# Kernel tuning notes

Hardware: AMD Instinct MI355X
Metric: run time of the kernel (lower is better)

## Reference

```python
import jax, jax.numpy as jnp
import numpy as np

N_NODES = 50000
N_EDGES = 800000
D_IN, D_HID, D_OUT = 256, 128, 64
NEG_SLOPE = 0.2  # PyG GATConv default


def gat_conv(x, W, a_src, a_dst, b, src, dst, n):
    """Single-head PyG-style GATConv with self-loops already in (src, dst)."""
    h = x @ W                                  # [N, d_out]
    # per-edge attention logits: LeakyReLU(a_src . h_src + a_dst . h_dst)
    e = jax.nn.leaky_relu((h @ a_src)[src] + (h @ a_dst)[dst], NEG_SLOPE)  # [E]
    # segment softmax over incoming edges of each dst node (stable)
    e = e - jax.ops.segment_max(e, dst, num_segments=n)[dst]
    p = jnp.exp(e)
    p = p / jax.ops.segment_sum(p, dst, num_segments=n)[dst]
    # weighted scatter-add of source messages
    out = jax.ops.segment_sum(p[:, None] * h[src], dst, num_segments=n)
    return out + b


def setup_inputs() -> dict:
    key = jax.random.key(0)
    ks = jax.random.split(key, 10)
    x = jax.random.normal(ks[0], (N_NODES, D_IN), dtype=jnp.float32)
    edge_index = jax.random.randint(ks[1], (2, N_EDGES), 0, N_NODES, dtype=jnp.int32)
    s1 = 1.0 / np.sqrt(D_IN)
    s2 = 1.0 / np.sqrt(D_HID)
    W1 = jax.random.normal(ks[2], (D_IN, D_HID), dtype=jnp.float32) * s1
    a_src1 = jax.random.normal(ks[3], (D_HID,), dtype=jnp.float32) * s2
    a_dst1 = jax.random.normal(ks[4], (D_HID,), dtype=jnp.float32) * s2
    b1 = jnp.zeros((D_HID,), dtype=jnp.float32)
    W2 = jax.random.normal(ks[5], (D_HID, D_OUT), dtype=jnp.float32) * s2
    a_src2 = jax.random.normal(ks[6], (D_OUT,), dtype=jnp.float32) * (1.0 / np.sqrt(D_OUT))
    a_dst2 = jax.random.normal(ks[7], (D_OUT,), dtype=jnp.float32) * (1.0 / np.sqrt(D_OUT))
    b2 = jnp.zeros((D_OUT,), dtype=jnp.float32)
    return {"x": x, "edge_index": edge_index, "W1": W1, "a_src1": a_src1,
            "a_dst1": a_dst1, "b1": b1, "W2": W2, "a_src2": a_src2,
            "a_dst2": a_dst2, "b2": b2}


def reference(x, edge_index, W1, a_src1, a_dst1, b1, W2, a_src2, a_dst2, b2):
    n = x.shape[0]
    loops = jnp.arange(n, dtype=edge_index.dtype)
    src = jnp.concatenate([edge_index[0], loops])  # add_self_loops=True (PyG default)
    dst = jnp.concatenate([edge_index[1], loops])
    h = gat_conv(x, W1, a_src1, a_dst1, b1, src, dst, n)
    h = jax.nn.relu(h)
    return gat_conv(h, W2, a_src2, a_dst2, b2, src, dst, n)
```

## Files before the change

kernel.cpp:

```cpp
#include <hip/hip_runtime.h>
#include <stdint.h>

#define DIN 256
#define DHID 128
#define DOUTD 64
#define NBLK 128
#define BCAP 4096

typedef __attribute__((ext_vector_type(8))) short bf16x8;
typedef __attribute__((ext_vector_type(4))) float f32x4;

__device__ __forceinline__ uint32_t pack_bf16x2(float x, float y) {
    uint32_t ux = __builtin_bit_cast(uint32_t, x);
    uint32_t uy = __builtin_bit_cast(uint32_t, y);
    ux += 0x7fffu + ((ux >> 16) & 1u);
    uy += 0x7fffu + ((uy >> 16) & 1u);
    return (ux >> 16) | (uy & 0xffff0000u);
}
__device__ __forceinline__ uint16_t to_bf16(float x) {
    uint32_t u = __builtin_bit_cast(uint32_t, x);
    u += 0x7fffu + ((u >> 16) & 1u);
    return (uint16_t)(u >> 16);
}
__device__ __forceinline__ float bflo(uint32_t v) { return __builtin_bit_cast(float, v << 16); }
__device__ __forceinline__ float bfhi(uint32_t v) { return __builtin_bit_cast(float, v & 0xffff0000u); }

template<int K, int N>
__device__ __forceinline__ void prepack_body(
    const float* __restrict__ W, uint16_t* __restrict__ Bp, int t)
{
    constexpr int CB = N / 16;
    if (t >= (K / 32) * CB * 64) return;
    const int lane = t & 63, fi = t >> 6;
    const int c = fi % CB, kb = fi / CB;
    const int j  = 16 * c + (lane & 15);
    const int k0 = kb * 32 + (lane >> 4) * 8;
    uint32_t o[4];
    #pragma unroll
    for (int i = 0; i < 4; ++i) {
        float lo = W[(size_t)(k0 + 2 * i)     * N + j];
        float hi = W[(size_t)(k0 + 2 * i + 1) * N + j];
        o[i] = pack_bf16x2(lo, hi);
    }
    *reinterpret_cast<uint4*>(&Bp[(size_t)t * 8]) = make_uint4(o[0], o[1], o[2], o[3]);
}

__global__ __launch_bounds__(256) void prepack_both_kernel(
    const float* __restrict__ W1, uint16_t* __restrict__ Bp1,
    const float* __restrict__ W2, uint16_t* __restrict__ Bp2,
    int* __restrict__ cntG, int nbuck)
{
    if (blockIdx.x == 0) {
        for (int i = threadIdx.x; i < nbuck; i += 256) cntG[i] = 0;
    }
    if (blockIdx.x < 16)
        prepack_body<DIN, DHID>(W1, Bp1, blockIdx.x * 256 + threadIdx.x);
    else
        prepack_body<DHID, DOUTD>(W2, Bp2, (blockIdx.x - 16) * 256 + threadIdx.x);
}

template<int K, int N, bool AF32>
__global__ __launch_bounds__(256) void mfma_gemm(
    const void* __restrict__ A, const uint16_t* __restrict__ Bp,
    uint16_t* __restrict__ Cout, const float* __restrict__ a_s,
    const float* __restrict__ a_d, float* __restrict__ asrc,
    float* __restrict__ adst, int M)
{
    constexpr int KB = K / 32, CB = N / 16;
    __shared__ __align__(16) uint16_t As[64 * K];

    const int tid = threadIdx.x;
    const int row0 = blockIdx.x * 64;

    if (AF32) {
        constexpr int NIT = 64 * K / 4 / 256;
        #pragma unroll
        for (int i = 0; i < NIT; ++i) {
            int u = tid + i * 256;
            int row = u / (K / 4);
            int k4  = (u % (K / 4)) * 4;
            float4 v = make_float4(0.f, 0.f, 0.f, 0.f);
            if (row0 + row < M)
                v = *reinterpret_cast<const float4*>((const float*)A + (size_t)(row0 + row) * K + k4);
            uint32_t byte = (uint32_t)row * (K * 2) + k4 * 2;
            byte ^= (row & 7) << 4;
            *reinterpret_cast<uint2*>((char*)As + byte) =
                make_uint2(pack_bf16x2(v.x, v.y), pack_bf16x2(v.z, v.w));
        }
    } else {
        constexpr int NIT = 64 * K / 8 / 256;
        #pragma unroll
        for (int i = 0; i < NIT; ++i) {
            int u = tid + i * 256;
            int row = u / (K / 8);
            int k8  = (u % (K / 8)) * 8;
            uint4 v = make_uint4(0u, 0u, 0u, 0u);
            if (row0 + row < M)
                v = *reinterpret_cast<const uint4*>((const uint16_t*)A + (size_t)(row0 + row) * K + k8);
            uint32_t byte = (uint32_t)row * (K * 2) + k8 * 2;
            byte ^= (row & 7) << 4;
            *reinterpret_cast<uint4*>((char*)As + byte) = v;
        }
    }
    __syncthreads();

    const int w = tid >> 6, l = tid & 63;
    const int rA = w * 16 + (l & 15);

    f32x4 acc[CB] = {};
    const char* blane = (const char*)Bp + l * 16;

    #pragma unroll
    for (int kb = 0; kb < KB; ++kb) {
        uint32_t abyte = (uint32_t)rA * (K * 2) + (kb * 32 + (l >> 4) * 8) * 2;
        abyte ^= (rA & 7) << 4;
        bf16x8 a = *reinterpret_cast<const bf16x8*>((const char*)As + abyte);
        #pragma unroll
        for (int c = 0; c < CB; ++c) {
            bf16x8 b = *reinterpret_cast<const bf16x8*>(blane + (size_t)(kb * CB + c) * 1024);
            acc[c] = __builtin_amdgcn_mfma_f32_16x16x32_bf16(a, b, acc[c], 0, 0, 0);
        }
    }

    const int rb = w * 16 + (l >> 4) * 4;
    const int colb = l & 15;

    #pragma unroll
    for (int c = 0; c < CB; ++c) {
        #pragma unroll
        for (int r = 0; r < 4; ++r) {
            int grow = row0 + rb + r;
            if (grow < M)
                Cout[(size_t)grow * N + c * 16 + colb] = to_bf16(acc[c][r]);
        }
    }

    float ps[4] = {}, pd[4] = {};
    #pragma unroll
    for (int c = 0; c < CB; ++c) {
        float asv = a_s[c * 16 + colb];
        float adv = a_d[c * 16 + colb];
        #pragma unroll
        for (int r = 0; r < 4; ++r) {
            ps[r] += acc[c][r] * asv;
            pd[r] += acc[c][r] * adv;
        }
    }
    #pragma unroll
    for (int mask = 1; mask < 16; mask <<= 1) {
        #pragma unroll
        for (int r = 0; r < 4; ++r) {
            ps[r] += __shfl_xor(ps[r], mask);
            pd[r] += __shfl_xor(pd[r], mask);
        }
    }
    if (colb == 0) {
        #pragma unroll
        for (int r = 0; r < 4; ++r) {
            int grow = row0 + rb + r;
            if (grow < M) { asrc[grow] = ps[r]; adst[grow] = pd[r]; }
        }
    }
}

__global__ __launch_bounds__(256) void histscatter_kernel(
    const int* __restrict__ ei, int E, int n, int nbuck, int chunk,
    int* __restrict__ cntG, uint32_t* __restrict__ bucketed)
{
    __shared__ int h[512];
    __shared__ int curL[512];
    for (int i = threadIdx.x; i < nbuck; i += 256) h[i] = 0;
    __syncthreads();
    const int blk = blockIdx.x;
    const int ET = E + n;
    const int e0 = blk * chunk, e1 = min(e0 + chunk, ET);
    for (int e = e0 + threadIdx.x; e < e1; e += 256) {
        int d = (e < E) ? ei[E + e] : (e - E);
        atomicAdd(&h[d >> 7], 1);
    }
    __syncthreads();
    for (int i = threadIdx.x; i < nbuck; i += 256) {
        int c = h[i];
        int base = i * BCAP;
        if (c) base += atomicAdd(&cntG[i], c);
        curL[i] = base;
    }
    __syncthreads();
    for (int e = e0 + threadIdx.x; e < e1; e += 256) {
        int s, d;
        if (e < E) { s = ei[e]; d = ei[E + e]; }
        else       { s = e - E; d = s; }
        int pos = atomicAdd(&curL[d >> 7], 1);
        bucketed[pos] = ((uint32_t)d << 16) | (uint32_t)s;
    }
}

__global__ __launch_bounds__(256) void csrF_kernel(
    const uint32_t* __restrict__ bucketed, const int* __restrict__ cntG,
    int n, int* __restrict__ offs, int* __restrict__ degs, int* __restrict__ csr)
{
    __shared__ int hist[128];
    __shared__ int scn[128];
    __shared__ int cur[128];
    const int b = blockIdx.x;
    const int tid = threadIdx.x;
    const int beg = b * BCAP;
    const int end = beg + cntG[b];

    if (tid < 128) hist[tid] = 0;
    __syncthreads();
    for (int i = beg + tid; i < end; i += 256)
        atomicAdd(&hist[(bucketed[i] >> 16) & 127], 1);
    __syncthreads();
    if (tid < 128) scn[tid] = hist[tid];
    __syncthreads();
    #pragma unroll
    for (int off = 1; off < 128; off <<= 1) {
        int v = (tid < 128 && tid >= off) ? scn[tid - off] : 0;
        __syncthreads();
        if (tid < 128) scn[tid] += v;
        __syncthreads();
    }
    if (tid < 128) {
        int excl = (tid == 0) ? 0 : scn[tid - 1];
        cur[tid] = beg + excl;
        int node = b * 128 + tid;
        if (node < n) { offs[node] = beg + excl; degs[node] = hist[tid]; }
    }
    __syncthreads();
    for (int i = beg + tid; i < end; i += 256) {
        uint32_t pk = bucketed[i];
        int pos = atomicAdd(&cur[(pk >> 16) & 127], 1);
        csr[pos] = (int)(pk & 0xFFFFu);
    }
}

template<int D, bool RELU, bool OUTB16>
__global__ __launch_bounds__(256) void agg_kernel(
    const uint32_t* __restrict__ Hb, const float* __restrict__ asrc,
    const float* __restrict__ adst, const int* __restrict__ offs,
    const int* __restrict__ degs, const int* __restrict__ csr_src,
    const float* __restrict__ bias, void* __restrict__ out, int n)
{
    constexpr int C16 = D / 8;
    constexpr int EPI = 64 / C16;
    const int wid = threadIdx.x >> 6, lane = threadIdx.x & 63;
    const int node = blockIdx.x * 4 + wid;
    if (node >= n) return;

    const int beg = offs[node];
    const int deg = degs[node];
    const float ad = adst[node];
    const int seg = lane / C16;
    const int chk = lane & (C16 - 1);
    const uint4* __restrict__ H4 = reinterpret_cast<const uint4*>(Hb);

    float acc[8] = {};
    float ssum = 0.f;

    for (int base = 0; base < deg; base += 64) {
        const int lim = min(64, deg - base);
        float wt = 0.f; int st = 0;
        if (lane < lim) {
            st = csr_src[beg + base + lane];
            float t = asrc[st] + ad;
            t = (t > 0.f) ? t : 0.2f * t;
            wt = __expf(t);
        }
        ssum += wt;
        const int iters = (lim + 2 * EPI - 1) / (2 * EPI);
        #pragma unroll 2
        for (int it = 0; it < iters; ++it) {
            int e0 = it * 2 * EPI + seg;
            int e1 = e0 + EPI;
            float w0 = __shfl(wt, e0);
            int   s0 = __shfl(st, e0);
            float w1 = __shfl(wt, e1);
            int   s1 = __shfl(st, e1);
            uint4 v0 = H4[(size_t)s0 * (D / 8) + chk];
            uint4 v1 = H4[(size_t)s1 * (D / 8) + chk];
            acc[0] += w0 * bflo(v0.x); acc[1] += w0 * bfhi(v0.x);
            acc[2] += w0 * bflo(v0.y); acc[3] += w0 * bfhi(v0.y);
            acc[4] += w0 * bflo(v0.z); acc[5] += w0 * bfhi(v0.z);
            acc[6] += w0 * bflo(v0.w); acc[7] += w0 * bfhi(v0.w);
            acc[0] += w1 * bflo(v1.x); acc[1] += w1 * bfhi(v1.x);
            acc[2] += w1 * bflo(v1.y); acc[3] += w1 * bfhi(v1.y);
            acc[4] += w1 * bflo(v1.z); acc[5] += w1 * bfhi(v1.z);
            acc[6] += w1 * bflo(v1.w); acc[7] += w1 * bfhi(v1.w);
        }
    }

    #pragma unroll
    for (int mask = C16; mask < 64; mask <<= 1)
        #pragma unroll
        for (int j = 0; j < 8; ++j)
            acc[j] += __shfl_xor(acc[j], mask);
    #pragma unroll
    for (int off = 32; off; off >>= 1) ssum += __shfl_xor(ssum, off);
    const float inv = 1.f / ssum;

    if (seg == 0) {
        const int col0 = chk * 8;
        float r[8];
        #pragma unroll
        for (int j = 0; j < 8; ++j) {
            r[j] = acc[j] * inv + bias[col0 + j];
            if (RELU) r[j] = fmaxf(r[j], 0.f);
        }
        if (OUTB16) {
            uint4 o = make_uint4(pack_bf16x2(r[0], r[1]), pack_bf16x2(r[2], r[3]),
                                 pack_bf16x2(r[4], r[5]), pack_bf16x2(r[6], r[7]));
            *(reinterpret_cast<uint4*>(out) + (size_t)node * (D / 8) + chk) = o;
        } else {
            float* op = (float*)out + (size_t)node * D + col0;
            *reinterpret_cast<float4*>(op)     = make_float4(r[0], r[1], r[2], r[3]);
            *reinterpret_cast<float4*>(op + 4) = make_float4(r[4], r[5], r[6], r[7]);
        }
    }
}

extern "C" void kernel_launch(void* const* d_in, const int* in_sizes, int n_in,
                              void* d_out, int out_size, void* d_ws, size_t ws_size,
                              hipStream_t stream)
{
    const float* x   = (const float*)d_in[0];
    const int*   ei  = (const int*)  d_in[1];
    const float* W1  = (const float*)d_in[2];
    const float* as1 = (const float*)d_in[3];
    const float* ad1 = (const float*)d_in[4];
    const float* b1  = (const float*)d_in[5];
    const float* W2  = (const float*)d_in[6];
    const float* as2 = (const float*)d_in[7];
    const float* ad2 = (const float*)d_in[8];
    const float* b2  = (const float*)d_in[9];
    float* out = (float*)d_out;

    const int n  = in_sizes[0] / DIN;
    const int E  = in_sizes[1] / 2;
    const int ET = E + n;

    const int nbuck  = (n + 127) >> 7;
    const int chunk  = (ET + NBLK - 1) / NBLK;

    char* ws = (char*)d_ws;
    size_t off = 0;
    auto alloc = [&](size_t bytes) -> void* {
        off = (off + 255) & ~(size_t)255;
        void* p = ws + off;
        off += bytes;
        return p;
    };
    uint16_t* Hb   = (uint16_t*)alloc((size_t)n * DHID * 2);
    uint16_t* O1b  = (uint16_t*)alloc((size_t)n * DHID * 2);
    uint16_t* H2b  = (uint16_t*)alloc((size_t)n * DOUTD * 2);
    float* asrc    = (float*)alloc((size_t)n * 4);
    float* adst    = (float*)alloc((size_t)n * 4);
    uint16_t* Bp1  = (uint16_t*)alloc((size_t)DIN * DHID * 2);
    uint16_t* Bp2  = (uint16_t*)alloc((size_t)DHID * DOUTD * 2);
    int* cntG  = (int*)alloc((size_t)nbuck * 4);
    int* offs  = (int*)alloc((size_t)n * 4);
    int* degs  = (int*)alloc((size_t)n * 4);
    uint32_t* bucketed = (uint32_t*)alloc((size_t)nbuck * BCAP * 4);
    int* csr   = (int*)alloc((size_t)nbuck * BCAP * 4);

    const int nw = (n + 3) / 4;
    const int ng = (n + 63) / 64;

    prepack_both_kernel<<<20, 256, 0, stream>>>(W1, Bp1, W2, Bp2, cntG, nbuck);

    histscatter_kernel<<<NBLK, 256, 0, stream>>>(ei, E, n, nbuck, chunk, cntG, bucketed);
    csrF_kernel<<<nbuck, 256, 0, stream>>>(bucketed, cntG, n, offs, degs, csr);

    mfma_gemm<DIN, DHID, true><<<ng, 256, 0, stream>>>(x, Bp1, Hb, as1, ad1, asrc, adst, n);
    agg_kernel<DHID, true, true><<<nw, 256, 0, stream>>>(
        (const uint32_t*)Hb, asrc, adst, offs, degs, csr, b1, O1b, n);

    mfma_gemm<DHID, DOUTD, false><<<ng, 256, 0, stream>>>(O1b, Bp2, H2b, as2, ad2, asrc, adst, n);
    agg_kernel<DOUTD, false, false><<<nw, 256, 0, stream>>>(
        (const uint32_t*)H2b, asrc, adst, offs, degs, csr, b2, out, n);
}
```

Baseline: 221.5 us.

## Fuse edge bucketing with layer-1 GEMM and build per-bucket CSR inside aggregation

The edge histogram/scatter pass and the first dense GEMM now run as one hybrid launch, with blocks split by index, so the two independent stages can overlap on the device. The separate CSR-finalize kernel is removed. Each aggregation block of 1024 threads instead sorts its 128-node bucket into a shared-memory CSR of 16-bit source indices, then processes those nodes with 16 waves. This cuts launches and global CSR/offset/degree traffic, and the local sort is repeated for both layers. It trades node-level parallelism in aggregation for larger blocks, fewer of them (about 391), and heavier LDS use, and the 16-bit indices cap the source id range.

```diff
diff --git a/kernel.cpp b/kernel.cpp
--- a/kernel.cpp
+++ b/kernel.cpp
@@ -60,17 +60,16 @@
 }
 
 template<int K, int N, bool AF32>
-__global__ __launch_bounds__(256) void mfma_gemm(
+__device__ __forceinline__ void gemm_body(
+    uint16_t* __restrict__ As,
     const void* __restrict__ A, const uint16_t* __restrict__ Bp,
     uint16_t* __restrict__ Cout, const float* __restrict__ a_s,
     const float* __restrict__ a_d, float* __restrict__ asrc,
-    float* __restrict__ adst, int M)
+    float* __restrict__ adst, int M, int bid)
 {
     constexpr int KB = K / 32, CB = N / 16;
-    __shared__ __align__(16) uint16_t As[64 * K];
-
     const int tid = threadIdx.x;
-    const int row0 = blockIdx.x * 64;
+    const int row0 = bid * 64;
 
     if (AF32) {
         constexpr int NIT = 64 * K / 4 / 256;
@@ -163,54 +162,84 @@
     }
 }
 
-__global__ __launch_bounds__(256) void histscatter_kernel(
+__global__ __launch_bounds__(256) void hybrid_kernel(
     const int* __restrict__ ei, int E, int n, int nbuck, int chunk,
-    int* __restrict__ cntG, uint32_t* __restrict__ bucketed)
-{
+    int* __restrict__ cntG, uint32_t* __restrict__ bucketed,
+    const float* __restrict__ x, const uint16_t* __restrict__ Bp1,
+    uint16_t* __restrict__ Hb, const float* __restrict__ a_s,
+    const float* __restrict__ a_d, float* __restrict__ asrc,
+    float* __restrict__ adst)
+{
+    __shared__ __align__(16) uint16_t As[64 * DIN];
     __shared__ int h[512];
     __shared__ int curL[512];
-    for (int i = threadIdx.x; i < nbuck; i += 256) h[i] = 0;
-    __syncthreads();
-    const int blk = blockIdx.x;
-    const int ET = E + n;
-    const int e0 = blk * chunk, e1 = min(e0 + chunk, ET);
-    for (int e = e0 + threadIdx.x; e < e1; e += 256) {
-        int d = (e < E) ? ei[E + e] : (e - E);
-        atomicAdd(&h[d >> 7], 1);
-    }
-    __syncthreads();
-    for (int i = threadIdx.x; i < nbuck; i += 256) {
-        int c = h[i];
-        int base = i * BCAP;
-        if (c) base += atomicAdd(&cntG[i], c);
-        curL[i] = base;
-    }
-    __syncthreads();
-    for (int e = e0 + threadIdx.x; e < e1; e += 256) {
-        int s, d;
-        if (e < E) { s = ei[e]; d = ei[E + e]; }
-        else       { s = e - E; d = s; }
-        int pos = atomicAdd(&curL[d >> 7], 1);
-        bucketed[pos] = ((uint32_t)d << 16) | (uint32_t)s;
-    }
-}
-
-__global__ __launch_bounds__(256) void csrF_kernel(
+
+    if (blockIdx.x < NBLK) {
+        for (int i = threadIdx.x; i < nbuck; i += 256) h[i] = 0;
+        __syncthreads();
+        const int blk = blockIdx.x;
+        const int ET = E + n;
+        const int e0 = blk * chunk, e1 = min(e0 + chunk, ET);
+        for (int e = e0 + threadIdx.x; e < e1; e += 256) {
+            int d = (e < E) ? ei[E + e] : (e - E);
+            atomicAdd(&h[d >> 7], 1);
+        }
+        __syncthreads();
+        for (int i = threadIdx.x; i < nbuck; i += 256) {
+            int c = h[i];
+            int base = i * BCAP;
+            if (c) base += atomicAdd(&cntG[i], c);
+            curL[i] = base;
+        }
+        __syncthreads();
+        for (int e = e0 + threadIdx.x; e < e1; e += 256) {
+            int s, d;
+            if (e < E) { s = ei[e]; d = ei[E + e]; }
+            else       { s = e - E; d = s; }
+            int pos = atomicAdd(&curL[d >> 7], 1);
+            bucketed[pos] = ((uint32_t)d << 16) | (uint32_t)s;
+        }
+    } else {
+        gemm_body<DIN, DHID, true>(As, x, Bp1, Hb, a_s, a_d, asrc, adst, n,
+                                   blockIdx.x - NBLK);
+    }
+}
+
+__global__ __launch_bounds__(256) void gemm2_kernel(
+    const uint16_t* __restrict__ A, const uint16_t* __restrict__ Bp,
+    uint16_t* __restrict__ Cout, const float* __restrict__ a_s,
+    const float* __restrict__ a_d, float* __restrict__ asrc,
+    float* __restrict__ adst, int M)
+{
+    __shared__ __align__(16) uint16_t As[64 * DHID];
+    gemm_body<DHID, DOUTD, false>(As, A, Bp, Cout, a_s, a_d, asrc, adst, M,
+                                  blockIdx.x);
+}
+
+template<int D, bool RELU, bool OUTB16>
+__global__ __launch_bounds__(1024) void aggF_kernel(
     const uint32_t* __restrict__ bucketed, const int* __restrict__ cntG,
-    int n, int* __restrict__ offs, int* __restrict__ degs, int* __restrict__ csr)
-{
+    const uint32_t* __restrict__ Hb, const float* __restrict__ asrc,
+    const float* __restrict__ adst, const float* __restrict__ bias,
+    void* __restrict__ out, int n)
+{
+    constexpr int C16 = D / 8;
+    constexpr int EPI = 64 / C16;
+    __shared__ uint16_t csr_l[BCAP];
     __shared__ int hist[128];
     __shared__ int scn[128];
+    __shared__ int offs_l[128];
     __shared__ int cur[128];
+
     const int b = blockIdx.x;
     const int tid = threadIdx.x;
-    const int beg = b * BCAP;
-    const int end = beg + cntG[b];
+    const int bbase = b * BCAP;
+    const int cnt = cntG[b];
 
     if (tid < 128) hist[tid] = 0;
     __syncthreads();
-    for (int i = beg + tid; i < end; i += 256)
-        atomicAdd(&hist[(bucketed[i] >> 16) & 127], 1);
+    for (int i = tid; i < cnt; i += 1024)
+        atomicAdd(&hist[(bucketed[bbase + i] >> 16) & 127], 1);
     __syncthreads();
     if (tid < 128) scn[tid] = hist[tid];
     __syncthreads();
@@ -222,99 +251,92 @@
         __syncthreads();
     }
     if (tid < 128) {
-        int excl = (tid == 0) ? 0 : scn[tid - 1];
-        cur[tid] = beg + excl;
-        int node = b * 128 + tid;
-        if (node < n) { offs[node] = beg + excl; degs[node] = hist[tid]; }
-    }
-    __syncthreads();
-    for (int i = beg + tid; i < end; i += 256) {
-        uint32_t pk = bucketed[i];
+        int excl = scn[tid] - hist[tid];
+        offs_l[tid] = excl;
+        cur[tid] = excl;
+    }
+    __syncthreads();
+    for (int i = tid; i < cnt; i += 1024) {
+        uint32_t pk = bucketed[bbase + i];
         int pos = atomicAdd(&cur[(pk >> 16) & 127], 1);
-        csr[pos] = (int)(pk & 0xFFFFu);
-    }
-}
-
-template<int D, bool RELU, bool OUTB16>
-__global__ __launch_bounds__(256) void agg_kernel(
-    const uint32_t* __restrict__ Hb, const float* __restrict__ asrc,
-    const float* __restrict__ adst, const int* __restrict__ offs,
-    const int* __restrict__ degs, const int* __restrict__ csr_src,
-    const float* __restrict__ bias, void* __restrict__ out, int n)
-{
-    constexpr int C16 = D / 8;
-    constexpr int EPI = 64 / C16;
-    const int wid = threadIdx.x >> 6, lane = threadIdx.x & 63;
-    const int node = blockIdx.x * 4 + wid;
-    if (node >= n) return;
-
-    const int beg = offs[node];
-    const int deg = degs[node];
-    const float ad = adst[node];
+        csr_l[pos] = (uint16_t)(pk & 0xFFFFu);
+    }
+    __syncthreads();
+
+    const int wv = tid >> 6, lane = tid & 63;
     const int seg = lane / C16;
     const int chk = lane & (C16 - 1);
     const uint4* __restrict__ H4 = reinterpret_cast<const uint4*>(Hb);
 
-    float acc[8] = {};
-    float ssum = 0.f;
-
-    for (int base = 0; base < deg; base += 64) {
-        const int lim = min(64, deg - base);
-        float wt = 0.f; int st = 0;
-        if (lane < lim) {
-            st = csr_src[beg + base + lane];
-            float t = asrc[st] + ad;
-            t = (t > 0.f) ? t : 0.2f * t;
-            wt = __expf(t);
-        }
-        ssum += wt;
-        const int iters = (lim + 2 * EPI - 1) / (2 * EPI);
-        #pragma unroll 2
-        for (int it = 0; it < iters; ++it) {
-            int e0 = it * 2 * EPI + seg;
-            int e1 = e0 + EPI;
-            float w0 = __shfl(wt, e0);
-            int   s0 = __shfl(st, e0);
-            float w1 = __shfl(wt, e1);
-            int   s1 = __shfl(st, e1);
-            uint4 v0 = H4[(size_t)s0 * (D / 8) + chk];
-            uint4 v1 = H4[(size_t)s1 * (D / 8) + chk];
-            acc[0] += w0 * bflo(v0.x); acc[1] += w0 * bfhi(v0.x);
-            acc[2] += w0 * bflo(v0.y); acc[3] += w0 * bfhi(v0.y);
-            acc[4] += w0 * bflo(v0.z); acc[5] += w0 * bfhi(v0.z);
-            acc[6] += w0 * bflo(v0.w); acc[7] += w0 * bfhi(v0.w);
-            acc[0] += w1 * bflo(v1.x); acc[1] += w1 * bfhi(v1.x);
-            acc[2] += w1 * bflo(v1.y); acc[3] += w1 * bfhi(v1.y);
-            acc[4] += w1 * bflo(v1.z); acc[5] += w1 * bfhi(v1.z);
-            acc[6] += w1 * bflo(v1.w); acc[7] += w1 * bfhi(v1.w);
-        }
-    }
-
-    #pragma unroll
-    for (int mask = C16; mask < 64; mask <<= 1)
-        #pragma unroll
-        for (int j = 0; j < 8; ++j)
-            acc[j] += __shfl_xor(acc[j], mask);
-    #pragma unroll
-    for (int off = 32; off; off >>= 1) ssum += __shfl_xor(ssum, off);
-    const float inv = 1.f / ssum;
-
-    if (seg == 0) {
-        const int col0 = chk * 8;
-        float r[8];
-        #pragma unroll
-        for (int j = 0; j < 8; ++j) {
-            r[j] = acc[j] * inv + bias[col0 + j];
-            if (RELU) r[j] = fmaxf(r[j], 0.f);
-        }
-        if (OUTB16) {
-            uint4 o = make_uint4(pack_bf16x2(r[0], r[1]), pack_bf16x2(r[2], r[3]),
-                                 pack_bf16x2(r[4], r[5]), pack_bf16x2(r[6], r[7]));
-            *(reinterpret_cast<uint4*>(out) + (size_t)node * (D / 8) + chk) = o;
-        } else {
-            float* op = (float*)out + (size_t)node * D + col0;
-            *reinterpret_cast<float4*>(op)     = make_float4(r[0], r[1], r[2], r[3]);
-            *reinterpret_cast<float4*>(op + 4) = make_float4(r[4], r[5], r[6], r[7]);
+    for (int j = 0; j < 8; ++j) {
+        const int ln = wv + 16 * j;
+        const int node = b * 128 + ln;
+        if (node >= n) continue;
+        const int beg = offs_l[ln];
+        const int deg = hist[ln];
+        const float ad = adst[node];
+
+        float acc[8] = {};
+        float ssum = 0.f;
+
+        for (int base = 0; base < deg; base += 64) {
+            const int lim = min(64, deg - base);
+            float wt = 0.f; int st = 0;
+            if (lane < lim) {
+                st = csr_l[beg + base + lane];
+                float t = asrc[st] + ad;
+                t = (t > 0.f) ? t : 0.2f * t;
+                wt = __expf(t);
+            }
+            ssum += wt;
+            const int iters = (lim + 2 * EPI - 1) / (2 * EPI);
+            #pragma unroll 2
+            for (int it = 0; it < iters; ++it) {
+                int e0 = it * 2 * EPI + seg;
+                int e1 = e0 + EPI;
+                float w0 = __shfl(wt, e0);
+                int   s0 = __shfl(st, e0);
+                float w1 = __shfl(wt, e1);
+                int   s1 = __shfl(st, e1);
+                uint4 v0 = H4[(size_t)s0 * (D / 8) + chk];
+                uint4 v1 = H4[(size_t)s1 * (D / 8) + chk];
+                acc[0] += w0 * bflo(v0.x); acc[1] += w0 * bfhi(v0.x);
+                acc[2] += w0 * bflo(v0.y); acc[3] += w0 * bfhi(v0.y);
+                acc[4] += w0 * bflo(v0.z); acc[5] += w0 * bfhi(v0.z);
+                acc[6] += w0 * bflo(v0.w); acc[7] += w0 * bfhi(v0.w);
+                acc[0] += w1 * bflo(v1.x); acc[1] += w1 * bfhi(v1.x);
+                acc[2] += w1 * bflo(v1.y); acc[3] += w1 * bfhi(v1.y);
+                acc[4] += w1 * bflo(v1.z); acc[5] += w1 * bfhi(v1.z);
+                acc[6] += w1 * bflo(v1.w); acc[7] += w1 * bfhi(v1.w);
+            }
+        }
+
+        #pragma unroll
+        for (int mask = C16; mask < 64; mask <<= 1)
+            #pragma unroll
+            for (int q = 0; q < 8; ++q)
+                acc[q] += __shfl_xor(acc[q], mask);
+        #pragma unroll
+        for (int off = 32; off; off >>= 1) ssum += __shfl_xor(ssum, off);
+        const float inv = 1.f / ssum;
+
+        if (seg == 0) {
+            const int col0 = chk * 8;
+            float r[8];
+            #pragma unroll
+            for (int q = 0; q < 8; ++q) {
+                r[q] = acc[q] * inv + bias[col0 + q];
+                if (RELU) r[q] = fmaxf(r[q], 0.f);
+            }
+            if (OUTB16) {
+                uint4 o = make_uint4(pack_bf16x2(r[0], r[1]), pack_bf16x2(r[2], r[3]),
+                                     pack_bf16x2(r[4], r[5]), pack_bf16x2(r[6], r[7]));
+                *(reinterpret_cast<uint4*>(out) + (size_t)node * (D / 8) + chk) = o;
+            } else {
+                float* op = (float*)out + (size_t)node * D + col0;
+                *reinterpret_cast<float4*>(op)     = make_float4(r[0], r[1], r[2], r[3]);
+                *reinterpret_cast<float4*>(op + 4) = make_float4(r[4], r[5], r[6], r[7]);
+            }
         }
     }
 }
@@ -358,24 +380,21 @@
     uint16_t* Bp1  = (uint16_t*)alloc((size_t)DIN * DHID * 2);
     uint16_t* Bp2  = (uint16_t*)alloc((size_t)DHID * DOUTD * 2);
     int* cntG  = (int*)alloc((size_t)nbuck * 4);
-    int* offs  = (int*)alloc((size_t)n * 4);
-    int* degs  = (int*)alloc((size_t)n * 4);
     uint32_t* bucketed = (uint32_t*)alloc((size_t)nbuck * BCAP * 4);
-    int* csr   = (int*)alloc((size_t)nbuck * BCAP * 4);
-
-    const int nw = (n + 3) / 4;
+
     const int ng = (n + 63) / 64;
 
     prepack_both_kernel<<<20, 256, 0, stream>>>(W1, Bp1, W2, Bp2, cntG, nbuck);
 
-    histscatter_kernel<<<NBLK, 256, 0, stream>>>(ei, E, n, nbuck, chunk, cntG, bucketed);
-    csrF_kernel<<<nbuck, 256, 0, stream>>>(bucketed, cntG, n, offs, degs, csr);
-
-    mfma_gemm<DIN, DHID, true><<<ng, 256, 0, stream>>>(x, Bp1, Hb, as1, ad1, asrc, adst, n);
-    agg_kernel<DHID, true, true><<<nw, 256, 0, stream>>>(
-        (const uint32_t*)Hb, asrc, adst, offs, degs, csr, b1, O1b, n);
-
-    mfma_gemm<DHID, DOUTD, false><<<ng, 256, 0, stream>>>(O1b, Bp2, H2b, as2, ad2, asrc, adst, n);
-    agg_kernel<DOUTD, false, false><<<nw, 256, 0, stream>>>(
-        (const uint32_t*)H2b, asrc, adst, offs, degs, csr, b2, out, n);
-}
+    hybrid_kernel<<<NBLK + ng, 256, 0, stream>>>(
+        ei, E, n, nbuck, chunk, cntG, bucketed,
+        x, Bp1, Hb, as1, ad1, asrc, adst);
+
+    aggF_kernel<DHID, true, true><<<nbuck, 1024, 0, stream>>>(
+        bucketed, cntG, (const uint32_t*)Hb, asrc, adst, b1, O1b, n);
+
+    gemm2_kernel<<<ng, 256, 0, stream>>>(O1b, Bp2, H2b, as2, ad2, asrc, adst, n);
+
+    aggF_kernel<DOUTD, false, false><<<nbuck, 1024, 0, stream>>>(
+        bucketed, cntG, (const uint32_t*)H2b, asrc, adst, b2, out, n);
+}
```

New measurement: 209.4 us. -5.5%, faster.
